# Optimization experiments

Hardware: AMD Instinct MI355X
Metric: run time of the kernel (lower is better)

## Reference

```python
import jax, jax.numpy as jnp
import numpy as np

T, E, DIM, HID = 8192, 8, 1024, 2048


def setup_inputs() -> dict:
    key = jax.random.key(0)
    k1, k2, k3 = jax.random.split(key, 3)
    x = jax.random.normal(k1, (T, DIM), dtype=jnp.float32)
    w1 = jax.random.normal(k2, (E, HID, DIM), dtype=jnp.float32)
    w2 = jax.random.normal(k3, (E, DIM, HID), dtype=jnp.float32)
    # Tokens are pre-grouped by expert; counts must sum exactly to T.
    num_tokens_per_expert = jnp.full((E,), T // E, dtype=jnp.int32)
    return {"x": x, "w1": w1, "w2": w2, "num_tokens_per_expert": num_tokens_per_expert}


def reference(x, w1, w2, num_tokens_per_expert):
    # Faithful to torch._grouped_mm path: bf16 casts, two ragged grouped GEMMs,
    # result cast back to x.dtype.
    gs = num_tokens_per_expert.astype(jnp.int32)
    xb = x.astype(jnp.bfloat16)                                  # [T, dim]
    w1t = jnp.swapaxes(w1.astype(jnp.bfloat16), -2, -1)          # [E, dim, hid]
    w2t = jnp.swapaxes(w2.astype(jnp.bfloat16), -2, -1)          # [E, hid, dim]
    h = jax.lax.ragged_dot(xb, w1t, gs)                          # [T, hid] bf16
    out = jax.lax.ragged_dot(h, w2t, gs)                         # [T, dim] bf16
    return out.astype(x.dtype)
```

## Files before the change

### kernel.cpp

```cpp
#include <hip/hip_runtime.h>
#include <stdint.h>

#define T_TOK 8192
#define NEXP  8
#define DIMSZ 1024
#define HIDSZ 2048

typedef __attribute__((ext_vector_type(4))) float f32x4;
typedef __attribute__((ext_vector_type(8))) short s16x8;


__device__ __forceinline__ uint16_t f2bf(float f) {
  uint32_t u = __builtin_bit_cast(uint32_t, f);
  u += 0x7fffu + ((u >> 16) & 1u);
  return (uint16_t)(u >> 16);
}

__device__ __forceinline__ void gload_lds16(const uint16_t* g, const uint16_t* lds_base) {
  __builtin_amdgcn_global_load_lds(
      (const __attribute__((address_space(1))) uint32_t*)(uintptr_t)g,
      (__attribute__((address_space(3))) uint32_t*)(uint32_t)(uintptr_t)lds_base,
      16, 0, 0);
}


__global__ void cvt_all(const float* __restrict__ x, const float* __restrict__ w1,
                        const float* __restrict__ w2, uint16_t* __restrict__ xb,
                        uint16_t* __restrict__ w1b, uint16_t* __restrict__ w2b,
                        const int* __restrict__ counts, int* __restrict__ offs,
                        int* __restrict__ toffs) {
  if (blockIdx.x == 0 && threadIdx.x == 0) {
    int s = 0, ts = 0;
    for (int e = 0; e < NEXP; ++e) {
      offs[e] = s; toffs[e] = ts;
      s += counts[e]; ts += (counts[e] + 127) >> 7;
    }
    offs[NEXP] = s; toffs[NEXP] = ts;
  }
  const int NX = (T_TOK * DIMSZ) / 16;
  const int NW = (NEXP * HIDSZ * DIMSZ) / 16;
  const int total = NX + 2 * NW;
  const int stride = gridDim.x * blockDim.x;
  for (int i = blockIdx.x * blockDim.x + threadIdx.x; i < total; i += stride) {
    const float* src; uint16_t* dst; int j;
    if (i < NX)           { src = x;  dst = xb;  j = i; }
    else if (i < NX + NW) { src = w1; dst = w1b; j = i - NX; }
    else                  { src = w2; dst = w2b; j = i - NX - NW; }
    const float4* p = (const float4*)src + 4 * (size_t)j;
    float4 a = p[0], b = p[1], c = p[2], d = p[3];
    uint4 o0, o1;
    o0.x = f2bf(a.x) | ((uint32_t)f2bf(a.y) << 16);
    o0.y = f2bf(a.z) | ((uint32_t)f2bf(a.w) << 16);
    o0.z = f2bf(b.x) | ((uint32_t)f2bf(b.y) << 16);
    o0.w = f2bf(b.z) | ((uint32_t)f2bf(b.w) << 16);
    o1.x = f2bf(c.x) | ((uint32_t)f2bf(c.y) << 16);
    o1.y = f2bf(c.z) | ((uint32_t)f2bf(c.w) << 16);
    o1.z = f2bf(d.x) | ((uint32_t)f2bf(d.y) << 16);
    o1.w = f2bf(d.z) | ((uint32_t)f2bf(d.w) << 16);
    uint4* q = (uint4*)dst + 2 * (size_t)j;
    q[0] = o0;
    q[1] = o1;
  }
}

template <bool OUT_BF16>
__global__ __launch_bounds__(256, 3)
void gemm_grouped(const uint16_t* __restrict__ A, const uint16_t* __restrict__ B,
                  void* __restrict__ C, const int* __restrict__ offs,
                  const int* __restrict__ toffs, int N, int K, int lognt) {
  __shared__ __align__(16) uint16_t As[128 * 64];
  __shared__ __align__(16) uint16_t Bs[128 * 64];

  const int mtg = blockIdx.x >> lognt;
  const int nt  = blockIdx.x & ((1 << lognt) - 1);
  if (mtg >= toffs[NEXP]) return;
  int e = 0;
#pragma unroll
  for (int i = 1; i < NEXP; ++i) e += (toffs[i] <= mtg) ? 1 : 0;
  const int mt      = mtg - toffs[e];
  const int m_start = offs[e];
  const int m_count = offs[e + 1] - m_start;
  const int m0      = mt * 128;
  int valid_m = m_count - m0;
  if (valid_m > 128) valid_m = 128;
  const int n0 = nt * 128;

  const int tid  = threadIdx.x;
  const int w    = tid >> 6;
  const int lane = tid & 63;
  const int wm = w & 1, wn = w >> 1;

  const uint16_t* gA = A + (size_t)m_start * K;
  const uint16_t* gB = B + (size_t)e * N * K;

  const uint16_t* ap[4];
  const uint16_t* bp[4];
#pragma unroll
  for (int c = 0; c < 4; ++c) {
    const int r  = w * 32 + c * 8 + (lane >> 3);
    const int q8 = ((lane & 7) ^ ((r >> 1) & 7)) * 8;
    const int ra = (r < valid_m) ? r : (valid_m - 1);
    ap[c] = gA + (size_t)(m0 + ra) * K + q8;
    bp[c] = gB + (size_t)(n0 + r) * K + q8;
  }

  const int fr = lane & 15;
  const int f0 = ((lane >> 4) ^ ((fr >> 1) & 7)) * 8;

  f32x4 acc[4][4];
#pragma unroll
  for (int mi = 0; mi < 4; ++mi)
#pragma unroll
    for (int ni = 0; ni < 4; ++ni) acc[mi][ni] = (f32x4){0.f, 0.f, 0.f, 0.f};

  for (int k0 = 0; k0 < K; k0 += 64) {
    __syncthreads();
#pragma unroll
    for (int c = 0; c < 4; ++c) {
      gload_lds16(ap[c], &As[(w * 32 + c * 8) * 64]);
      gload_lds16(bp[c], &Bs[(w * 32 + c * 8) * 64]);
    }
#pragma unroll
    for (int c = 0; c < 4; ++c) { ap[c] += 64; bp[c] += 64; }
    __syncthreads();

#pragma unroll
    for (int kk = 0; kk < 2; ++kk) {
      const int fk = f0 ^ (kk << 5);
      s16x8 af[4], bf[4];
#pragma unroll
      for (int mi = 0; mi < 4; ++mi)
        af[mi] = *(const s16x8*)&As[(wm * 64 + mi * 16 + fr) * 64 + fk];
#pragma unroll
      for (int ni = 0; ni < 4; ++ni)
        bf[ni] = *(const s16x8*)&Bs[(wn * 64 + ni * 16 + fr) * 64 + fk];
#pragma unroll
      for (int mi = 0; mi < 4; ++mi)
#pragma unroll
        for (int ni = 0; ni < 4; ++ni)
          acc[mi][ni] = __builtin_amdgcn_mfma_f32_16x16x32_bf16(af[mi], bf[ni], acc[mi][ni], 0, 0, 0);
    }
  }

  const int cq = (lane >> 4) * 4;
  const int cc = lane & 15;
#pragma unroll
  for (int mi = 0; mi < 4; ++mi) {
#pragma unroll
    for (int r = 0; r < 4; ++r) {
      const int rt = wm * 64 + mi * 16 + cq + r;
      if (rt < valid_m) {
        const size_t rowoff = (size_t)(m_start + m0 + rt) * N;
#pragma unroll
        for (int ni = 0; ni < 4; ++ni) {
          const int col = n0 + wn * 64 + ni * 16 + cc;
          const float v = acc[mi][ni][r];
          if (OUT_BF16) {
            ((uint16_t*)C)[rowoff + col] = f2bf(v);
          } else {
            const uint32_t b = (uint32_t)f2bf(v) << 16;
            ((float*)C)[rowoff + col] = __builtin_bit_cast(float, b);
          }
        }
      }
    }
  }
}


extern "C" void kernel_launch(void* const* d_in, const int* in_sizes, int n_in,
                              void* d_out, int out_size, void* d_ws, size_t ws_size,
                              hipStream_t stream) {
  const float* x  = (const float*)d_in[0];
  const float* w1 = (const float*)d_in[1];
  const float* w2 = (const float*)d_in[2];
  const int* cnt  = (const int*)d_in[3];
  float* out = (float*)d_out;

  char* ws = (char*)d_ws;
  uint16_t* xb  = (uint16_t*)(ws);
  uint16_t* w1b = (uint16_t*)(ws + 16777216);
  uint16_t* w2b = (uint16_t*)(ws + 50331648);
  uint16_t* h   = (uint16_t*)(ws + 83886080);
  int* offs     = (int*)(ws + 117440512);
  int* toffs    = offs + 9;

  cvt_all<<<2048, 256, 0, stream>>>(x, w1, w2, xb, w1b, w2b, cnt, offs, toffs);

  const int MAX_MT = T_TOK / 128 + NEXP - 1;

  gemm_grouped<true><<<MAX_MT * 16, 256, 0, stream>>>(
      xb, w1b, (void*)h, offs, toffs, HIDSZ, DIMSZ, 4);

  gemm_grouped<false><<<MAX_MT * 8, 256, 0, stream>>>(
      h, w2b, (void*)out, offs, toffs, DIMSZ, HIDSZ, 3);
}
```

Before: 269.9 us.

## Fuse fp32-to-bf16 weight conversion into grouped GEMM B-tile loading

Drops the separate conversion pass for w1 and w2 and has each GEMM block load fp32 weight tiles directly, convert them to bf16 in registers and write them swizzled into LDS, with a one-iteration register prefetch. This removes a large standalone memory pass that read and rewrote both weight tensors. In exchange, weight tiles are read in fp32 by every M tile, doubling per-block B traffic, and B staging becomes synchronous register stores rather than async global-to-LDS loads. It also adds register pressure.

```diff
diff --git a/kernel.cpp b/kernel.cpp
--- a/kernel.cpp
+++ b/kernel.cpp
@@ -14,6 +14,10 @@
   uint32_t u = __builtin_bit_cast(uint32_t, f);
   u += 0x7fffu + ((u >> 16) & 1u);
   return (uint16_t)(u >> 16);
+}
+
+__device__ __forceinline__ uint32_t pkbf(float a, float b) {
+  return (uint32_t)f2bf(a) | ((uint32_t)f2bf(b) << 16);
 }
 
 __device__ __forceinline__ void gload_lds16(const uint16_t* g, const uint16_t* lds_base) {
@@ -24,11 +28,9 @@
 }
 
 
-__global__ void cvt_all(const float* __restrict__ x, const float* __restrict__ w1,
-                        const float* __restrict__ w2, uint16_t* __restrict__ xb,
-                        uint16_t* __restrict__ w1b, uint16_t* __restrict__ w2b,
-                        const int* __restrict__ counts, int* __restrict__ offs,
-                        int* __restrict__ toffs) {
+__global__ void cvt_x(const float* __restrict__ x, uint16_t* __restrict__ xb,
+                      const int* __restrict__ counts, int* __restrict__ offs,
+                      int* __restrict__ toffs) {
   if (blockIdx.x == 0 && threadIdx.x == 0) {
     int s = 0, ts = 0;
     for (int e = 0; e < NEXP; ++e) {
@@ -37,35 +39,22 @@
     }
     offs[NEXP] = s; toffs[NEXP] = ts;
   }
-  const int NX = (T_TOK * DIMSZ) / 16;
-  const int NW = (NEXP * HIDSZ * DIMSZ) / 16;
-  const int total = NX + 2 * NW;
-  const int stride = gridDim.x * blockDim.x;
-  for (int i = blockIdx.x * blockDim.x + threadIdx.x; i < total; i += stride) {
-    const float* src; uint16_t* dst; int j;
-    if (i < NX)           { src = x;  dst = xb;  j = i; }
-    else if (i < NX + NW) { src = w1; dst = w1b; j = i - NX; }
-    else                  { src = w2; dst = w2b; j = i - NX - NW; }
-    const float4* p = (const float4*)src + 4 * (size_t)j;
-    float4 a = p[0], b = p[1], c = p[2], d = p[3];
-    uint4 o0, o1;
-    o0.x = f2bf(a.x) | ((uint32_t)f2bf(a.y) << 16);
-    o0.y = f2bf(a.z) | ((uint32_t)f2bf(a.w) << 16);
-    o0.z = f2bf(b.x) | ((uint32_t)f2bf(b.y) << 16);
-    o0.w = f2bf(b.z) | ((uint32_t)f2bf(b.w) << 16);
-    o1.x = f2bf(c.x) | ((uint32_t)f2bf(c.y) << 16);
-    o1.y = f2bf(c.z) | ((uint32_t)f2bf(c.w) << 16);
-    o1.z = f2bf(d.x) | ((uint32_t)f2bf(d.y) << 16);
-    o1.w = f2bf(d.z) | ((uint32_t)f2bf(d.w) << 16);
-    uint4* q = (uint4*)dst + 2 * (size_t)j;
-    q[0] = o0;
-    q[1] = o1;
-  }
+  const size_t i = blockIdx.x * (size_t)blockDim.x + threadIdx.x;
+  const float4* p = (const float4*)x + 4 * i;
+  float4 a = p[0], b = p[1], c = p[2], d = p[3];
+  uint4 o0, o1;
+  o0.x = pkbf(a.x, a.y); o0.y = pkbf(a.z, a.w);
+  o0.z = pkbf(b.x, b.y); o0.w = pkbf(b.z, b.w);
+  o1.x = pkbf(c.x, c.y); o1.y = pkbf(c.z, c.w);
+  o1.z = pkbf(d.x, d.y); o1.w = pkbf(d.z, d.w);
+  uint4* q = (uint4*)xb + 2 * i;
+  q[0] = o0;
+  q[1] = o1;
 }
 
 template <bool OUT_BF16>
 __global__ __launch_bounds__(256, 3)
-void gemm_grouped(const uint16_t* __restrict__ A, const uint16_t* __restrict__ B,
+void gemm_grouped(const uint16_t* __restrict__ A, const float* __restrict__ B,
                   void* __restrict__ C, const int* __restrict__ offs,
                   const int* __restrict__ toffs, int N, int K, int lognt) {
   __shared__ __align__(16) uint16_t As[128 * 64];
@@ -91,17 +80,24 @@
   const int wm = w & 1, wn = w >> 1;
 
   const uint16_t* gA = A + (size_t)m_start * K;
-  const uint16_t* gB = B + (size_t)e * N * K;
+  const float*    gB = B + (size_t)e * N * K;
 
   const uint16_t* ap[4];
-  const uint16_t* bp[4];
 #pragma unroll
   for (int c = 0; c < 4; ++c) {
     const int r  = w * 32 + c * 8 + (lane >> 3);
     const int q8 = ((lane & 7) ^ ((r >> 1) & 7)) * 8;
     const int ra = (r < valid_m) ? r : (valid_m - 1);
     ap[c] = gA + (size_t)(m0 + ra) * K + q8;
-    bp[c] = gB + (size_t)(n0 + r) * K + q8;
+  }
+
+  const float* bp[4];
+  int bwoff[4];
+#pragma unroll
+  for (int c = 0; c < 4; ++c) {
+    const int r = w * 32 + c * 8 + (lane >> 3);
+    bp[c] = gB + (size_t)(n0 + r) * K + (lane & 7) * 8;
+    bwoff[c] = r * 64 + (((lane & 7) ^ ((r >> 1) & 7)) * 8);
   }
 
   const int fr = lane & 15;
@@ -113,16 +109,41 @@
 #pragma unroll
     for (int ni = 0; ni < 4; ++ni) acc[mi][ni] = (f32x4){0.f, 0.f, 0.f, 0.f};
 
+  float4 bq[8];
+#pragma unroll
+  for (int c = 0; c < 4; ++c) {
+    bq[2 * c]     = *(const float4*)bp[c];
+    bq[2 * c + 1] = *(const float4*)(bp[c] + 4);
+    bp[c] += 64;
+  }
+
   for (int k0 = 0; k0 < K; k0 += 64) {
     __syncthreads();
 #pragma unroll
     for (int c = 0; c < 4; ++c) {
       gload_lds16(ap[c], &As[(w * 32 + c * 8) * 64]);
-      gload_lds16(bp[c], &Bs[(w * 32 + c * 8) * 64]);
-    }
-#pragma unroll
-    for (int c = 0; c < 4; ++c) { ap[c] += 64; bp[c] += 64; }
+      ap[c] += 64;
+    }
+#pragma unroll
+    for (int c = 0; c < 4; ++c) {
+      uint4 o;
+      o.x = pkbf(bq[2 * c].x,     bq[2 * c].y);
+      o.y = pkbf(bq[2 * c].z,     bq[2 * c].w);
+      o.z = pkbf(bq[2 * c + 1].x, bq[2 * c + 1].y);
+      o.w = pkbf(bq[2 * c + 1].z, bq[2 * c + 1].w);
+      *(uint4*)&Bs[bwoff[c]] = o;
+    }
     __syncthreads();
+
+    if (k0 + 64 < K) {
+#pragma unroll
+      for (int c = 0; c < 4; ++c) {
+        bq[2 * c]     = *(const float4*)bp[c];
+        bq[2 * c + 1] = *(const float4*)(bp[c] + 4);
+        bp[c] += 64;
+      }
+    }
+    asm volatile("" ::: "memory");
 
 #pragma unroll
     for (int kk = 0; kk < 2; ++kk) {
@@ -178,20 +199,18 @@
   float* out = (float*)d_out;
 
   char* ws = (char*)d_ws;
-  uint16_t* xb  = (uint16_t*)(ws);
-  uint16_t* w1b = (uint16_t*)(ws + 16777216);
-  uint16_t* w2b = (uint16_t*)(ws + 50331648);
-  uint16_t* h   = (uint16_t*)(ws + 83886080);
-  int* offs     = (int*)(ws + 117440512);
-  int* toffs    = offs + 9;
-
-  cvt_all<<<2048, 256, 0, stream>>>(x, w1, w2, xb, w1b, w2b, cnt, offs, toffs);
+  uint16_t* xb = (uint16_t*)(ws);
+  uint16_t* h  = (uint16_t*)(ws + 16777216);
+  int* offs    = (int*)(ws + 50331648);
+  int* toffs   = offs + 9;
+
+  cvt_x<<<2048, 256, 0, stream>>>(x, xb, cnt, offs, toffs);
 
   const int MAX_MT = T_TOK / 128 + NEXP - 1;
 
   gemm_grouped<true><<<MAX_MT * 16, 256, 0, stream>>>(
-      xb, w1b, (void*)h, offs, toffs, HIDSZ, DIMSZ, 4);
+      xb, w1, (void*)h, offs, toffs, HIDSZ, DIMSZ, 4);
 
   gemm_grouped<false><<<MAX_MT * 8, 256, 0, stream>>>(
-      h, w2b, (void*)out, offs, toffs, DIMSZ, HIDSZ, 3);
-}
+      h, w2, (void*)out, offs, toffs, DIMSZ, HIDSZ, 3);
+}
```

After: 287.8 us. +6.6%, slower.

## Overlap w2 bf16 conversion with first GEMM and remap blocks per XCD

Applied to the files above, without the earlier changes.

Moves the fp32-to-bf16 conversion of w2 out of the initial conversion kernel and into 512 extra blocks prepended to the first grouped GEMM launch. That memory-bound conversion can then run alongside the compute-bound GEMM1 tiles instead of serialising before them. It also remaps GEMM block indices so that consecutive tiles land on the same XCD, for better L2 locality. In exchange, the conversion blocks take CU slots away from GEMM1 and the launch grows larger.

```diff
diff --git a/kernel.cpp b/kernel.cpp
--- a/kernel.cpp
+++ b/kernel.cpp
@@ -14,6 +14,24 @@
   uint32_t u = __builtin_bit_cast(uint32_t, f);
   u += 0x7fffu + ((u >> 16) & 1u);
   return (uint16_t)(u >> 16);
+}
+
+__device__ __forceinline__ uint32_t pkbf(float a, float b) {
+  return (uint32_t)f2bf(a) | ((uint32_t)f2bf(b) << 16);
+}
+
+__device__ __forceinline__ void cvt_unit(const float* __restrict__ src,
+                                         uint16_t* __restrict__ dst, size_t j) {
+  const float4* p = (const float4*)src + 4 * j;
+  float4 a = p[0], b = p[1], c = p[2], d = p[3];
+  uint4 o0, o1;
+  o0.x = pkbf(a.x, a.y); o0.y = pkbf(a.z, a.w);
+  o0.z = pkbf(b.x, b.y); o0.w = pkbf(b.z, b.w);
+  o1.x = pkbf(c.x, c.y); o1.y = pkbf(c.z, c.w);
+  o1.z = pkbf(d.x, d.y); o1.w = pkbf(d.z, d.w);
+  uint4* q = (uint4*)dst + 2 * j;
+  q[0] = o0;
+  q[1] = o1;
 }
 
 __device__ __forceinline__ void gload_lds16(const uint16_t* g, const uint16_t* lds_base) {
@@ -24,9 +42,8 @@
 }
 
 
-__global__ void cvt_all(const float* __restrict__ x, const float* __restrict__ w1,
-                        const float* __restrict__ w2, uint16_t* __restrict__ xb,
-                        uint16_t* __restrict__ w1b, uint16_t* __restrict__ w2b,
+__global__ void cvt_xw1(const float* __restrict__ x, const float* __restrict__ w1,
+                        uint16_t* __restrict__ xb, uint16_t* __restrict__ w1b,
                         const int* __restrict__ counts, int* __restrict__ offs,
                         int* __restrict__ toffs) {
   if (blockIdx.x == 0 && threadIdx.x == 0) {
@@ -39,27 +56,11 @@
   }
   const int NX = (T_TOK * DIMSZ) / 16;
   const int NW = (NEXP * HIDSZ * DIMSZ) / 16;
-  const int total = NX + 2 * NW;
+  const int total = NX + NW;
   const int stride = gridDim.x * blockDim.x;
   for (int i = blockIdx.x * blockDim.x + threadIdx.x; i < total; i += stride) {
-    const float* src; uint16_t* dst; int j;
-    if (i < NX)           { src = x;  dst = xb;  j = i; }
-    else if (i < NX + NW) { src = w1; dst = w1b; j = i - NX; }
-    else                  { src = w2; dst = w2b; j = i - NX - NW; }
-    const float4* p = (const float4*)src + 4 * (size_t)j;
-    float4 a = p[0], b = p[1], c = p[2], d = p[3];
-    uint4 o0, o1;
-    o0.x = f2bf(a.x) | ((uint32_t)f2bf(a.y) << 16);
-    o0.y = f2bf(a.z) | ((uint32_t)f2bf(a.w) << 16);
-    o0.z = f2bf(b.x) | ((uint32_t)f2bf(b.y) << 16);
-    o0.w = f2bf(b.z) | ((uint32_t)f2bf(b.w) << 16);
-    o1.x = f2bf(c.x) | ((uint32_t)f2bf(c.y) << 16);
-    o1.y = f2bf(c.z) | ((uint32_t)f2bf(c.w) << 16);
-    o1.z = f2bf(d.x) | ((uint32_t)f2bf(d.y) << 16);
-    o1.w = f2bf(d.z) | ((uint32_t)f2bf(d.w) << 16);
-    uint4* q = (uint4*)dst + 2 * (size_t)j;
-    q[0] = o0;
-    q[1] = o1;
+    if (i < NX) cvt_unit(x, xb, i);
+    else        cvt_unit(w1, w1b, i - NX);
   }
 }
 
@@ -67,12 +68,26 @@
 __global__ __launch_bounds__(256, 3)
 void gemm_grouped(const uint16_t* __restrict__ A, const uint16_t* __restrict__ B,
                   void* __restrict__ C, const int* __restrict__ offs,
-                  const int* __restrict__ toffs, int N, int K, int lognt) {
+                  const int* __restrict__ toffs, int N, int K, int lognt,
+                  const float* __restrict__ cvt_src, uint16_t* __restrict__ cvt_dst,
+                  int ncvt, int cvt_units) {
   __shared__ __align__(16) uint16_t As[128 * 64];
   __shared__ __align__(16) uint16_t Bs[128 * 64];
 
-  const int mtg = blockIdx.x >> lognt;
-  const int nt  = blockIdx.x & ((1 << lognt) - 1);
+  if (blockIdx.x < (unsigned)ncvt) {
+    const int cstride = ncvt * 256;
+    for (int u = blockIdx.x * 256 + threadIdx.x; u < cvt_units; u += cstride)
+      cvt_unit(cvt_src, cvt_dst, u);
+    return;
+  }
+
+  const int nb   = gridDim.x - ncvt;
+  const int orig = blockIdx.x - ncvt;
+  const int qc = nb >> 3, rc = nb & 7, xcd = orig & 7;
+  const int bid = (xcd < rc ? xcd * (qc + 1) : rc * (qc + 1) + (xcd - rc) * qc) + (orig >> 3);
+
+  const int mtg = bid >> lognt;
+  const int nt  = bid & ((1 << lognt) - 1);
   if (mtg >= toffs[NEXP]) return;
   int e = 0;
 #pragma unroll
@@ -185,13 +200,16 @@
   int* offs     = (int*)(ws + 117440512);
   int* toffs    = offs + 9;
 
-  cvt_all<<<2048, 256, 0, stream>>>(x, w1, w2, xb, w1b, w2b, cnt, offs, toffs);
+  cvt_xw1<<<2048, 256, 0, stream>>>(x, w1, xb, w1b, cnt, offs, toffs);
 
   const int MAX_MT = T_TOK / 128 + NEXP - 1;
-
-  gemm_grouped<true><<<MAX_MT * 16, 256, 0, stream>>>(
-      xb, w1b, (void*)h, offs, toffs, HIDSZ, DIMSZ, 4);
+  const int NCVT   = 512;
+  const int W2U    = (NEXP * DIMSZ * HIDSZ) / 16;
+
+  gemm_grouped<true><<<NCVT + MAX_MT * 16, 256, 0, stream>>>(
+      xb, w1b, (void*)h, offs, toffs, HIDSZ, DIMSZ, 4, w2, w2b, NCVT, W2U);
 
   gemm_grouped<false><<<MAX_MT * 8, 256, 0, stream>>>(
-      h, w2b, (void*)out, offs, toffs, DIMSZ, HIDSZ, 3);
-}
+      h, w2b, (void*)out, offs, toffs, DIMSZ, HIDSZ, 3, (const float*)nullptr,
+      (uint16_t*)nullptr, 0, 0);
+}
```

After: 277.9 us. +3.0%, slower.
